# Kernel optimization log

Measured on AMD Instinct MI355X. Metric: run time of the kernel, lower is better.

## Reference

```python
import jax, jax.numpy as jnp
import numpy as np

NUM_HEADS = 12
WINDOW = 7            # window_size (and window_pretrain)
MASK_WINDOWS = 64     # windows per image (56x56 feature map / 7x7 windows)
TABLE_SIZE = (2 * WINDOW - 1) ** 2  # 169


def setup_inputs() -> dict:
    key = jax.random.key(0)
    ks = jax.random.split(key, 8)
    B, L, C = 2048, WINDOW * WINDOW, 384
    x = jax.random.normal(ks[0], (B, L, C), jnp.float32)
    rel_index = jax.random.randint(ks[1], (L * L,), 0, TABLE_SIZE, jnp.int32)
    attn_mask = jax.random.normal(ks[2], (1, MASK_WINDOWS, 1, L, L), jnp.float32) * 0.05
    # learned params
    qkv_w = jax.random.normal(ks[3], (C, 3 * C), jnp.float32) * 0.02
    qkv_b = jnp.zeros((3 * C,), jnp.float32)
    rel_bias_table = jax.random.normal(ks[4], (TABLE_SIZE, NUM_HEADS), jnp.float32) * 0.02
    proj_w = jax.random.normal(ks[5], (C, C), jnp.float32) * 0.02
    proj_b = jnp.zeros((C,), jnp.float32)
    return {"x": x, "rel_index": rel_index, "attn_mask": attn_mask,
            "qkv_w": qkv_w, "qkv_b": qkv_b, "rel_bias_table": rel_bias_table,
            "proj_w": proj_w, "proj_b": proj_b}


def reference(x, rel_index, attn_mask, qkv_w, qkv_b, rel_bias_table, proj_w, proj_b):
    B, L, C = x.shape
    H = NUM_HEADS
    D = C // H
    scale = D ** -0.5
    # qkv projection -> [3, B, H, L, D]
    qkv = (x @ qkv_w + qkv_b).reshape(B, L, 3, H, D).transpose(2, 0, 3, 1, 4)
    q, k, v = qkv[0], qkv[1], qkv[2]
    attn = jnp.einsum('bhqd,bhkd->bhqk', q * scale, k)  # [B,H,L,L]
    # gathered relative position bias: [L*L, H] -> [H, L, L]
    bias = rel_bias_table[rel_index].reshape(L, L, H).transpose(2, 0, 1)
    attn = attn + bias[None]
    # shifted-window mask add (with_mask=True path)
    attn = attn.reshape(-1, MASK_WINDOWS, H, L, L) + attn_mask
    attn = attn.reshape(-1, H, L, L)
    attn = jax.nn.softmax(attn, axis=-1)
    out = jnp.einsum('bhqk,bhkd->bqhd', attn, v).reshape(B, L, C)
    return out @ proj_w + proj_b
```

## Files before the change

### kernel.cpp

```cpp
#include <hip/hip_runtime.h>

typedef _Float16 half8 __attribute__((ext_vector_type(8)));
typedef _Float16 half4v __attribute__((ext_vector_type(4)));
typedef float f32x4 __attribute__((ext_vector_type(4)));
typedef float f32x2 __attribute__((ext_vector_type(2)));

constexpr int NB = 2048;
constexpr int CDIM = 384;
constexpr int NH = 12;
constexpr int MM = NB * 49;
constexpr float SCALE = 0.17677669529663687f;

__device__ __forceinline__ void async16(const void* g, void* l) {
    __builtin_amdgcn_global_load_lds((const __attribute__((address_space(1))) void*)g,
                                     (__attribute__((address_space(3))) void*)l, 16, 0, 0);
}


__global__ __launch_bounds__(256) void convert_x(const float* __restrict__ x,
                                                 _Float16* __restrict__ o, int n) {
    int i = (blockIdx.x * 256 + threadIdx.x) * 4;
    if (i < n) {
        float4 v = *(const float4*)(x + i);
        half4v h = { (_Float16)v.x, (_Float16)v.y, (_Float16)v.z, (_Float16)v.w };
        *(half4v*)(o + i) = h;
    }
}

__global__ __launch_bounds__(256) void convert_w(const float* __restrict__ qkv_w,
                                                 const float* __restrict__ proj_w,
                                                 _Float16* __restrict__ qkvT,
                                                 _Float16* __restrict__ projT) {
    int i = blockIdx.x * 256 + threadIdx.x;
    if (i < 1152 * 384) {
        int n = i / 384, kk = i % 384;
        qkvT[i] = (_Float16)qkv_w[kk * 1152 + n];
    } else {
        int j = i - 1152 * 384;
        if (j < 384 * 384) {
            int n = j / 384, kk = j % 384;
            projT[j] = (_Float16)proj_w[kk * 384 + n];
        }
    }
}


__global__ __launch_bounds__(256) void build_ft(const int* __restrict__ rel_index,
                                                const float* __restrict__ rtable,
                                                const float* __restrict__ mask,
                                                float* __restrict__ FT) {
    int wh = blockIdx.x;
    int w = wh / 12, h = wh - w * 12;
    float* dst = FT + (size_t)wh * 4096;
    for (int idx = threadIdx.x; idx < 4096; idx += 256) {
        int k = idx >> 6, q = idx & 63;
        float v = 0.f;
        if (k < 49 && q < 49)
            v = rtable[rel_index[q * 49 + k] * NH + h] + mask[(size_t)w * 2401 + q * 49 + k];
        dst[idx] = v;
    }
}


__global__ __launch_bounds__(256) void gemm_qkv(const _Float16* __restrict__ A,
                                                const _Float16* __restrict__ Bt,
                                                const float* __restrict__ qkv_b,
                                                _Float16* __restrict__ qo,
                                                _Float16* __restrict__ ko,
                                                _Float16* __restrict__ vo) {
    __shared__ _Float16 As[128 * 64];
    __shared__ _Float16 Bs[128 * 64];
    const int K = 384;
    const int tn = blockIdx.x, tm = blockIdx.y;
    const int t = threadIdx.x;
    const int wave = t >> 6, lane = t & 63;
    const int wm = (wave & 1) * 64, wn = (wave >> 1) * 64;
    const int quad = lane >> 4, l16 = lane & 15;
    const int rsub = lane >> 3, p = lane & 7;

    f32x4 acc[4][4] = {};
    const _Float16* Abase = A + (size_t)(tm * 128) * K;
    const _Float16* Bbase = Bt + (size_t)(tn * 128) * K;

    for (int k0 = 0; k0 < K; k0 += 64) {
        __syncthreads();
#pragma unroll
        for (int n = 0; n < 4; n++) {
            int ni = wave * 4 + n;
            int row = ni * 8 + rsub;
            int chunk = p ^ (row & 7);
            async16(Abase + (size_t)row * K + k0 + chunk * 8, (char*)As + ni * 1024);
            async16(Bbase + (size_t)row * K + k0 + chunk * 8, (char*)Bs + ni * 1024);
        }
        __syncthreads();
#pragma unroll
        for (int ks = 0; ks < 2; ks++) {
            half8 af[4], bfv[4];
#pragma unroll
            for (int i = 0; i < 4; i++)
                af[i] = *(const half8*)(&As[(wm + i * 16 + l16) * 64 + (((ks * 4 + quad) ^ (l16 & 7)) * 8)]);
#pragma unroll
            for (int j = 0; j < 4; j++)
                bfv[j] = *(const half8*)(&Bs[(wn + j * 16 + l16) * 64 + (((ks * 4 + quad) ^ (l16 & 7)) * 8)]);
#pragma unroll
            for (int i = 0; i < 4; i++)
#pragma unroll
                for (int j = 0; j < 4; j++)
                    acc[i][j] = __builtin_amdgcn_mfma_f32_16x16x32_f16(af[i], bfv[j], acc[i][j], 0, 0, 0);
        }
    }

    const int mbase = tm * 128, nbase = tn * 128;
#pragma unroll
    for (int j = 0; j < 4; j++) {
        int n = nbase + wn + j * 16 + l16;
        float bias = qkv_b[n];
        int s = n / 384, rem = n % 384;
        int h = rem >> 5, d = rem & 31;
#pragma unroll
        for (int i = 0; i < 4; i++) {
#pragma unroll
            for (int r = 0; r < 4; r++) {
                int m = mbase + wm + i * 16 + quad * 4 + r;
                int b = m / 49, l = m - b * 49;
                float v = acc[i][j][r] + bias;
                size_t bh = (size_t)b * NH + h;
                if (s == 0)       qo[(bh * 49 + l) * 32 + d] = (_Float16)(v * SCALE);
                else if (s == 1)  ko[(bh * 49 + l) * 32 + d] = (_Float16)v;
                else              vo[(bh * 32 + d) * 64 + l] = (_Float16)v;
            }
        }
    }
}


__global__ __launch_bounds__(256) void attn_kernel(const _Float16* __restrict__ qg,
                                                   const _Float16* __restrict__ kg,
                                                   const _Float16* __restrict__ vg,
                                                   const float* __restrict__ FT,
                                                   _Float16* __restrict__ out) {
    __shared__ float Pb[2][4][16 * 66];
    const int t = threadIdx.x;
    const int wave = t >> 6, lane = t & 63, quad = lane >> 4, l16 = lane & 15;
    const int gw = blockIdx.x * 4 + wave;
    const int b = gw / 12, h = gw - b * 12;

    const _Float16* qb = qg + (size_t)gw * 49 * 32;
    const _Float16* kb = kg + (size_t)gw * 49 * 32;
    const _Float16* vb = vg + (size_t)gw * 32 * 64;
    const float* Fb = FT + ((size_t)((b & 63) * 12 + h)) * 4096;

    half8 bk[4], bv[2][2];
#pragma unroll
    for (int j = 0; j < 4; j++) {
        int krow = j * 16 + l16; if (krow > 48) krow = 48;
        bk[j] = *(const half8*)(kb + krow * 32 + quad * 8);
    }
#pragma unroll
    for (int nt = 0; nt < 2; nt++)
#pragma unroll
        for (int ks = 0; ks < 2; ks++)
            bv[nt][ks] = *(const half8*)(vb + (nt * 16 + l16) * 64 + ks * 32 + quad * 8);

#pragma unroll
    for (int i = 0; i < 4; i++) {
        int qrow = i * 16 + l16; if (qrow > 48) qrow = 48;
        half8 aq = *(const half8*)(qb + qrow * 32 + quad * 8);

        f32x4 acc[4];
#pragma unroll
        for (int j = 0; j < 4; j++)
            acc[j] = *(const f32x4*)(Fb + (j * 16 + l16) * 64 + i * 16 + quad * 4);
#pragma unroll
        for (int j = 0; j < 4; j++)
            acc[j] = __builtin_amdgcn_mfma_f32_16x16x32_f16(aq, bk[j], acc[j], 0, 0, 0);

        if (l16 != 0) {
#pragma unroll
            for (int r = 0; r < 4; r++) acc[3][r] = -1e30f;
        }

        float rinv[4];
#pragma unroll
        for (int r = 0; r < 4; r++) {
            float m = fmaxf(fmaxf(acc[0][r], acc[1][r]), fmaxf(acc[2][r], acc[3][r]));
            m = fmaxf(m, __shfl_xor(m, 1, 64));
            m = fmaxf(m, __shfl_xor(m, 2, 64));
            m = fmaxf(m, __shfl_xor(m, 4, 64));
            m = fmaxf(m, __shfl_xor(m, 8, 64));
            float s = 0.f;
#pragma unroll
            for (int j = 0; j < 4; j++) {
                float e = __expf(acc[j][r] - m);
                acc[j][r] = e;
                s += e;
            }
            s += __shfl_xor(s, 1, 64);
            s += __shfl_xor(s, 2, 64);
            s += __shfl_xor(s, 4, 64);
            s += __shfl_xor(s, 8, 64);
            rinv[r] = 1.f / s;
        }

        float* Pw = &Pb[i & 1][wave][0];
#pragma unroll
        for (int j = 0; j < 4; j++)
#pragma unroll
            for (int r = 0; r < 4; r++)
                Pw[(quad * 4 + r) * 66 + j * 16 + l16] = acc[j][r];
        __syncthreads();

        f32x4 oacc[2] = {};
#pragma unroll
        for (int ks = 0; ks < 2; ks++) {
            const float* pp = Pw + l16 * 66 + ks * 32 + quad * 8;
            f32x2 p0 = *(const f32x2*)(pp);
            f32x2 p1 = *(const f32x2*)(pp + 2);
            f32x2 p2 = *(const f32x2*)(pp + 4);
            f32x2 p3 = *(const f32x2*)(pp + 6);
            half8 ap = { (_Float16)p0.x, (_Float16)p0.y, (_Float16)p1.x, (_Float16)p1.y,
                         (_Float16)p2.x, (_Float16)p2.y, (_Float16)p3.x, (_Float16)p3.y };
#pragma unroll
            for (int nt = 0; nt < 2; nt++)
                oacc[nt] = __builtin_amdgcn_mfma_f32_16x16x32_f16(ap, bv[nt][ks], oacc[nt], 0, 0, 0);
        }

#pragma unroll
        for (int nt = 0; nt < 2; nt++)
#pragma unroll
            for (int r = 0; r < 4; r++) {
                int q = i * 16 + quad * 4 + r;
                if (q < 49)
                    out[((size_t)b * 49 + q) * 384 + h * 32 + nt * 16 + l16] =
                        (_Float16)(oacc[nt][r] * rinv[r]);
            }
    }
}


__global__ __launch_bounds__(256) void gemm_proj(const _Float16* __restrict__ A,
                                                 const _Float16* __restrict__ Bt,
                                                 const float* __restrict__ proj_b,
                                                 float* __restrict__ out) {
    __shared__ _Float16 As[128 * 64];
    __shared__ _Float16 Bs[128 * 64];
    const int K = 384;
    const int tn = blockIdx.x, tm = blockIdx.y;
    const int t = threadIdx.x;
    const int wave = t >> 6, lane = t & 63;
    const int wm = (wave & 1) * 64, wn = (wave >> 1) * 64;
    const int quad = lane >> 4, l16 = lane & 15;
    const int rsub = lane >> 3, p = lane & 7;

    f32x4 acc[4][4] = {};
    const _Float16* Abase = A + (size_t)(tm * 128) * K;
    const _Float16* Bbase = Bt + (size_t)(tn * 128) * K;

    for (int k0 = 0; k0 < K; k0 += 64) {
        __syncthreads();
#pragma unroll
        for (int n = 0; n < 4; n++) {
            int ni = wave * 4 + n;
            int row = ni * 8 + rsub;
            int chunk = p ^ (row & 7);
            async16(Abase + (size_t)row * K + k0 + chunk * 8, (char*)As + ni * 1024);
            async16(Bbase + (size_t)row * K + k0 + chunk * 8, (char*)Bs + ni * 1024);
        }
        __syncthreads();
#pragma unroll
        for (int ks = 0; ks < 2; ks++) {
            half8 af[4], bfv[4];
#pragma unroll
            for (int i = 0; i < 4; i++)
                af[i] = *(const half8*)(&As[(wm + i * 16 + l16) * 64 + (((ks * 4 + quad) ^ (l16 & 7)) * 8)]);
#pragma unroll
            for (int j = 0; j < 4; j++)
                bfv[j] = *(const half8*)(&Bs[(wn + j * 16 + l16) * 64 + (((ks * 4 + quad) ^ (l16 & 7)) * 8)]);
#pragma unroll
            for (int i = 0; i < 4; i++)
#pragma unroll
                for (int j = 0; j < 4; j++)
                    acc[i][j] = __builtin_amdgcn_mfma_f32_16x16x32_f16(af[i], bfv[j], acc[i][j], 0, 0, 0);
        }
    }

    const int mbase = tm * 128, nbase = tn * 128;
#pragma unroll
    for (int j = 0; j < 4; j++) {
        int n = nbase + wn + j * 16 + l16;
        float bias = proj_b[n];
#pragma unroll
        for (int i = 0; i < 4; i++) {
#pragma unroll
            for (int r = 0; r < 4; r++) {
                int m = mbase + wm + i * 16 + quad * 4 + r;
                out[(size_t)m * 384 + n] = acc[i][j][r] + bias;
            }
        }
    }
}


extern "C" void kernel_launch(void* const* d_in, const int* in_sizes, int n_in,
                              void* d_out, int out_size, void* d_ws, size_t ws_size,
                              hipStream_t stream) {
    const float* x        = (const float*)d_in[0];
    const int*   rel_idx  = (const int*)d_in[1];
    const float* amask    = (const float*)d_in[2];
    const float* qkv_w    = (const float*)d_in[3];
    const float* qkv_b    = (const float*)d_in[4];
    const float* rtable   = (const float*)d_in[5];
    const float* proj_w   = (const float*)d_in[6];
    const float* proj_b   = (const float*)d_in[7];
    float* out = (float*)d_out;

    char* w = (char*)d_ws;
    const size_t XB = (size_t)MM * CDIM * 2;
    const size_t VB = (size_t)NB * NH * 32 * 64 * 2;
    _Float16* x_h    = (_Float16*)w;
    _Float16* wqkvT  = (_Float16*)(w + XB);
    _Float16* wprojT = (_Float16*)(w + XB + 884736);
    char* base0 = w + XB + 884736 + 294912;
    _Float16* q_h = (_Float16*)(base0);
    _Float16* k_h = (_Float16*)(base0 + XB);
    _Float16* v_h = (_Float16*)(base0 + 2 * XB);
    float*    FT  = (float*)(base0 + 2 * XB + VB);
    _Float16* ao_h = x_h;

    int nx = MM * CDIM;
    convert_x<<<nx / 1024, 256, 0, stream>>>(x, x_h, nx);
    convert_w<<<(1152 * 384 + 384 * 384) / 256, 256, 0, stream>>>(qkv_w, proj_w, wqkvT, wprojT);
    build_ft<<<768, 256, 0, stream>>>(rel_idx, rtable, amask, FT);
    gemm_qkv<<<dim3(9, MM / 128), 256, 0, stream>>>(x_h, wqkvT, qkv_b, q_h, k_h, v_h);
    attn_kernel<<<NB * NH / 4, 256, 0, stream>>>(q_h, k_h, v_h, FT, ao_h);
    gemm_proj<<<dim3(3, MM / 128), 256, 0, stream>>>(ao_h, wprojT, proj_b, out);
}
```

Before: 705.4 us.

## Stage QKV epilogue through LDS for coalesced stores and merge prep kernels

The QKV GEMM epilogue now writes its tile into shared memory and then stores rows coalesced into a plain row-major [M,1152] buffer, replacing the scattered per-element q/k/v stores and the transposed V layout. The attention kernel reads Q/K with row stride 1152 and transposes V into LDS per wave. It also keeps the probability tile in fp16 per wave, which removes the block-wide __syncthreads and the double buffer. The three preprocessing kernels are merged into one launch. The trade is an extra LDS transpose and strided global reads inside attention in exchange for cheaper GEMM stores and fewer launches.

```diff
diff --git a/kernel.cpp b/kernel.cpp
--- a/kernel.cpp
+++ b/kernel.cpp
@@ -1,15 +1,17 @@
 #include <hip/hip_runtime.h>
 
 typedef _Float16 half8 __attribute__((ext_vector_type(8)));
-typedef _Float16 half4v __attribute__((ext_vector_type(4)));
 typedef float f32x4 __attribute__((ext_vector_type(4)));
-typedef float f32x2 __attribute__((ext_vector_type(2)));
 
 constexpr int NB = 2048;
 constexpr int CDIM = 384;
 constexpr int NH = 12;
 constexpr int MM = NB * 49;
+constexpr int NTOT = 1152;
 constexpr float SCALE = 0.17677669529663687f;
+
+constexpr int XBLK = 37632;
+constexpr int WBLK = 2304;
 
 __device__ __forceinline__ void async16(const void* g, void* l) {
     __builtin_amdgcn_global_load_lds((const __attribute__((address_space(1))) void*)g,
@@ -17,47 +19,44 @@
 }
 
 
-__global__ __launch_bounds__(256) void convert_x(const float* __restrict__ x,
-                                                 _Float16* __restrict__ o, int n) {
-    int i = (blockIdx.x * 256 + threadIdx.x) * 4;
-    if (i < n) {
+__global__ __launch_bounds__(256) void prep(const float* __restrict__ x,
+                                            const float* __restrict__ qkv_w,
+                                            const float* __restrict__ proj_w,
+                                            const int* __restrict__ rel_index,
+                                            const float* __restrict__ rtable,
+                                            const float* __restrict__ mask,
+                                            _Float16* __restrict__ x_h,
+                                            _Float16* __restrict__ qkvT,
+                                            _Float16* __restrict__ projT,
+                                            float* __restrict__ FT) {
+    int bid = blockIdx.x;
+    if (bid < XBLK) {
+        size_t i = ((size_t)bid * 256 + threadIdx.x) * 4;
         float4 v = *(const float4*)(x + i);
-        half4v h = { (_Float16)v.x, (_Float16)v.y, (_Float16)v.z, (_Float16)v.w };
-        *(half4v*)(o + i) = h;
-    }
-}
-
-__global__ __launch_bounds__(256) void convert_w(const float* __restrict__ qkv_w,
-                                                 const float* __restrict__ proj_w,
-                                                 _Float16* __restrict__ qkvT,
-                                                 _Float16* __restrict__ projT) {
-    int i = blockIdx.x * 256 + threadIdx.x;
-    if (i < 1152 * 384) {
-        int n = i / 384, kk = i % 384;
-        qkvT[i] = (_Float16)qkv_w[kk * 1152 + n];
-    } else {
-        int j = i - 1152 * 384;
-        if (j < 384 * 384) {
+        _Float16 h0 = (_Float16)v.x, h1 = (_Float16)v.y, h2 = (_Float16)v.z, h3 = (_Float16)v.w;
+        _Float16* o = x_h + i;
+        o[0] = h0; o[1] = h1; o[2] = h2; o[3] = h3;
+    } else if (bid < XBLK + WBLK) {
+        int i = (bid - XBLK) * 256 + threadIdx.x;
+        if (i < 1152 * 384) {
+            int n = i / 384, kk = i % 384;
+            qkvT[i] = (_Float16)qkv_w[kk * 1152 + n];
+        } else {
+            int j = i - 1152 * 384;
             int n = j / 384, kk = j % 384;
             projT[j] = (_Float16)proj_w[kk * 384 + n];
         }
-    }
-}
-
-
-__global__ __launch_bounds__(256) void build_ft(const int* __restrict__ rel_index,
-                                                const float* __restrict__ rtable,
-                                                const float* __restrict__ mask,
-                                                float* __restrict__ FT) {
-    int wh = blockIdx.x;
-    int w = wh / 12, h = wh - w * 12;
-    float* dst = FT + (size_t)wh * 4096;
-    for (int idx = threadIdx.x; idx < 4096; idx += 256) {
-        int k = idx >> 6, q = idx & 63;
-        float v = 0.f;
-        if (k < 49 && q < 49)
-            v = rtable[rel_index[q * 49 + k] * NH + h] + mask[(size_t)w * 2401 + q * 49 + k];
-        dst[idx] = v;
+    } else {
+        int wh = bid - XBLK - WBLK;
+        int w = wh / 12, h = wh - w * 12;
+        float* dst = FT + (size_t)wh * 4096;
+        for (int idx = threadIdx.x; idx < 4096; idx += 256) {
+            int k = idx >> 6, q = idx & 63;
+            float v = 0.f;
+            if (k < 49 && q < 49)
+                v = rtable[rel_index[q * 49 + k] * NH + h] + mask[(size_t)w * 2401 + q * 49 + k];
+            dst[idx] = v;
+        }
     }
 }
 
@@ -65,11 +64,14 @@
 __global__ __launch_bounds__(256) void gemm_qkv(const _Float16* __restrict__ A,
                                                 const _Float16* __restrict__ Bt,
                                                 const float* __restrict__ qkv_b,
-                                                _Float16* __restrict__ qo,
-                                                _Float16* __restrict__ ko,
-                                                _Float16* __restrict__ vo) {
-    __shared__ _Float16 As[128 * 64];
-    __shared__ _Float16 Bs[128 * 64];
+                                                _Float16* __restrict__ C) {
+    __shared__ union {
+        struct { _Float16 A[128 * 64]; _Float16 B[128 * 64]; } st;
+        _Float16 tile[128 * 136];
+    } sm;
+    _Float16* As = sm.st.A;
+    _Float16* Bs = sm.st.B;
+
     const int K = 384;
     const int tn = blockIdx.x, tm = blockIdx.y;
     const int t = threadIdx.x;
@@ -110,62 +112,89 @@
         }
     }
 
-    const int mbase = tm * 128, nbase = tn * 128;
+    __syncthreads();
+    const int nbase = tn * 128, mbase = tm * 128;
+    const float s = (tn < 3) ? SCALE : 1.f;
+    float bj[4];
+#pragma unroll
+    for (int j = 0; j < 4; j++) bj[j] = qkv_b[nbase + wn + j * 16 + l16];
+
 #pragma unroll
     for (int j = 0; j < 4; j++) {
-        int n = nbase + wn + j * 16 + l16;
-        float bias = qkv_b[n];
-        int s = n / 384, rem = n % 384;
-        int h = rem >> 5, d = rem & 31;
+        int n = wn + j * 16 + l16;
 #pragma unroll
         for (int i = 0; i < 4; i++) {
 #pragma unroll
             for (int r = 0; r < 4; r++) {
-                int m = mbase + wm + i * 16 + quad * 4 + r;
-                int b = m / 49, l = m - b * 49;
-                float v = acc[i][j][r] + bias;
-                size_t bh = (size_t)b * NH + h;
-                if (s == 0)       qo[(bh * 49 + l) * 32 + d] = (_Float16)(v * SCALE);
-                else if (s == 1)  ko[(bh * 49 + l) * 32 + d] = (_Float16)v;
-                else              vo[(bh * 32 + d) * 64 + l] = (_Float16)v;
+                int m = wm + i * 16 + quad * 4 + r;
+                sm.tile[m * 136 + n] = (_Float16)((acc[i][j][r] + bj[j]) * s);
             }
         }
     }
-}
-
-
-__global__ __launch_bounds__(256) void attn_kernel(const _Float16* __restrict__ qg,
-                                                   const _Float16* __restrict__ kg,
-                                                   const _Float16* __restrict__ vg,
+    __syncthreads();
+
+    const int rcol = (t & 15) * 8;
+    const int rrow0 = t >> 4;
+#pragma unroll
+    for (int g = 0; g < 8; g++) {
+        int row = g * 16 + rrow0;
+        half8 val = *(const half8*)(&sm.tile[row * 136 + rcol]);
+        *(half8*)(C + (size_t)(mbase + row) * NTOT + nbase + rcol) = val;
+    }
+}
+
+
+__global__ __launch_bounds__(256) void attn_kernel(const _Float16* __restrict__ C,
                                                    const float* __restrict__ FT,
                                                    _Float16* __restrict__ out) {
-    __shared__ float Pb[2][4][16 * 66];
+    __shared__ _Float16 Vt[4][32 * 72];
+    __shared__ _Float16 Pb[4][16 * 72];
     const int t = threadIdx.x;
     const int wave = t >> 6, lane = t & 63, quad = lane >> 4, l16 = lane & 15;
     const int gw = blockIdx.x * 4 + wave;
     const int b = gw / 12, h = gw - b * 12;
 
-    const _Float16* qb = qg + (size_t)gw * 49 * 32;
-    const _Float16* kb = kg + (size_t)gw * 49 * 32;
-    const _Float16* vb = vg + (size_t)gw * 32 * 64;
+    const _Float16* qb = C + (size_t)b * 49 * NTOT + h * 32;
+    const _Float16* kb = qb + 384;
+    const _Float16* vb = qb + 768;
     const float* Fb = FT + ((size_t)((b & 63) * 12 + h)) * 4096;
 
-    half8 bk[4], bv[2][2];
+    _Float16* vt = Vt[wave];
+    {
+        int d = lane >> 1, seg = lane & 1;
+        half8 z = {};
+        *(half8*)(&vt[d * 72 + 48 + seg * 8]) = z;
+    }
+#pragma unroll
+    for (int i2 = 0; i2 < 4; i2++) {
+        int l = i2 * 16 + (lane >> 2);
+        int d0 = (lane & 3) * 8;
+        if (l < 49) {
+            half8 v8 = *(const half8*)(vb + (size_t)l * NTOT + d0);
+#pragma unroll
+            for (int e = 0; e < 8; e++)
+                vt[(d0 + e) * 72 + l] = v8[e];
+        }
+    }
+
+    half8 bk[4];
 #pragma unroll
     for (int j = 0; j < 4; j++) {
         int krow = j * 16 + l16; if (krow > 48) krow = 48;
-        bk[j] = *(const half8*)(kb + krow * 32 + quad * 8);
-    }
+        bk[j] = *(const half8*)(kb + (size_t)krow * NTOT + quad * 8);
+    }
+    half8 bv[2][2];
 #pragma unroll
     for (int nt = 0; nt < 2; nt++)
 #pragma unroll
         for (int ks = 0; ks < 2; ks++)
-            bv[nt][ks] = *(const half8*)(vb + (nt * 16 + l16) * 64 + ks * 32 + quad * 8);
-
+            bv[nt][ks] = *(const half8*)(&vt[(nt * 16 + l16) * 72 + ks * 32 + quad * 8]);
+
+    _Float16* Pw = Pb[wave];
 #pragma unroll
     for (int i = 0; i < 4; i++) {
         int qrow = i * 16 + l16; if (qrow > 48) qrow = 48;
-        half8 aq = *(const half8*)(qb + qrow * 32 + quad * 8);
+        half8 aq = *(const half8*)(qb + (size_t)qrow * NTOT + quad * 8);
 
         f32x4 acc[4];
 #pragma unroll
@@ -188,38 +217,30 @@
             m = fmaxf(m, __shfl_xor(m, 2, 64));
             m = fmaxf(m, __shfl_xor(m, 4, 64));
             m = fmaxf(m, __shfl_xor(m, 8, 64));
-            float s = 0.f;
+            float sum = 0.f;
 #pragma unroll
             for (int j = 0; j < 4; j++) {
                 float e = __expf(acc[j][r] - m);
                 acc[j][r] = e;
-                s += e;
+                sum += e;
             }
-            s += __shfl_xor(s, 1, 64);
-            s += __shfl_xor(s, 2, 64);
-            s += __shfl_xor(s, 4, 64);
-            s += __shfl_xor(s, 8, 64);
-            rinv[r] = 1.f / s;
-        }
-
-        float* Pw = &Pb[i & 1][wave][0];
+            sum += __shfl_xor(sum, 1, 64);
+            sum += __shfl_xor(sum, 2, 64);
+            sum += __shfl_xor(sum, 4, 64);
+            sum += __shfl_xor(sum, 8, 64);
+            rinv[r] = 1.f / sum;
+        }
+
 #pragma unroll
         for (int j = 0; j < 4; j++)
 #pragma unroll
             for (int r = 0; r < 4; r++)
-                Pw[(quad * 4 + r) * 66 + j * 16 + l16] = acc[j][r];
-        __syncthreads();
+                Pw[(quad * 4 + r) * 72 + j * 16 + l16] = (_Float16)acc[j][r];
 
         f32x4 oacc[2] = {};
 #pragma unroll
         for (int ks = 0; ks < 2; ks++) {
-            const float* pp = Pw + l16 * 66 + ks * 32 + quad * 8;
-            f32x2 p0 = *(const f32x2*)(pp);
-            f32x2 p1 = *(const f32x2*)(pp + 2);
-            f32x2 p2 = *(const f32x2*)(pp + 4);
-            f32x2 p3 = *(const f32x2*)(pp + 6);
-            half8 ap = { (_Float16)p0.x, (_Float16)p0.y, (_Float16)p1.x, (_Float16)p1.y,
-                         (_Float16)p2.x, (_Float16)p2.y, (_Float16)p3.x, (_Float16)p3.y };
+            half8 ap = *(const half8*)(&Pw[l16 * 72 + ks * 32 + quad * 8]);
 #pragma unroll
             for (int nt = 0; nt < 2; nt++)
                 oacc[nt] = __builtin_amdgcn_mfma_f32_16x16x32_f16(ap, bv[nt][ks], oacc[nt], 0, 0, 0);
@@ -231,7 +252,7 @@
             for (int r = 0; r < 4; r++) {
                 int q = i * 16 + quad * 4 + r;
                 if (q < 49)
-                    out[((size_t)b * 49 + q) * 384 + h * 32 + nt * 16 + l16] =
+                    out[((size_t)b * 49 + q) * CDIM + h * 32 + nt * 16 + l16] =
                         (_Float16)(oacc[nt][r] * rinv[r]);
             }
     }
@@ -294,7 +315,7 @@
 #pragma unroll
             for (int r = 0; r < 4; r++) {
                 int m = mbase + wm + i * 16 + quad * 4 + r;
-                out[(size_t)m * 384 + n] = acc[i][j][r] + bias;
+                out[(size_t)m * CDIM + n] = acc[i][j][r] + bias;
             }
         }
     }
@@ -316,22 +337,17 @@
 
     char* w = (char*)d_ws;
     const size_t XB = (size_t)MM * CDIM * 2;
-    const size_t VB = (size_t)NB * NH * 32 * 64 * 2;
+    const size_t CB = (size_t)MM * NTOT * 2;
     _Float16* x_h    = (_Float16*)w;
     _Float16* wqkvT  = (_Float16*)(w + XB);
     _Float16* wprojT = (_Float16*)(w + XB + 884736);
-    char* base0 = w + XB + 884736 + 294912;
-    _Float16* q_h = (_Float16*)(base0);
-    _Float16* k_h = (_Float16*)(base0 + XB);
-    _Float16* v_h = (_Float16*)(base0 + 2 * XB);
-    float*    FT  = (float*)(base0 + 2 * XB + VB);
-    _Float16* ao_h = x_h;
-
-    int nx = MM * CDIM;
-    convert_x<<<nx / 1024, 256, 0, stream>>>(x, x_h, nx);
-    convert_w<<<(1152 * 384 + 384 * 384) / 256, 256, 0, stream>>>(qkv_w, proj_w, wqkvT, wprojT);
-    build_ft<<<768, 256, 0, stream>>>(rel_idx, rtable, amask, FT);
-    gemm_qkv<<<dim3(9, MM / 128), 256, 0, stream>>>(x_h, wqkvT, qkv_b, q_h, k_h, v_h);
-    attn_kernel<<<NB * NH / 4, 256, 0, stream>>>(q_h, k_h, v_h, FT, ao_h);
+    _Float16* Cbuf   = (_Float16*)(w + XB + 884736 + 294912);
+    float*    FT     = (float*)(w + XB + 884736 + 294912 + CB);
+    _Float16* ao_h   = x_h;
+
+    prep<<<XBLK + WBLK + 768, 256, 0, stream>>>(x, qkv_w, proj_w, rel_idx, rtable, amask,
+                                                x_h, wqkvT, wprojT, FT);
+    gemm_qkv<<<dim3(9, MM / 128), 256, 0, stream>>>(x_h, wqkvT, qkv_b, Cbuf);
+    attn_kernel<<<NB * NH / 4, 256, 0, stream>>>(Cbuf, FT, ao_h);
     gemm_proj<<<dim3(3, MM / 128), 256, 0, stream>>>(ao_h, wprojT, proj_b, out);
 }
```

Result: faster. 626.9 us (-11.1%).
